# Kernel tuning notes

Measured on AMD Instinct MI355X. Metric: run time of the kernel, lower is better.

## Reference

```python
import jax, jax.numpy as jnp
import numpy as np
from jax import lax

H = 1024
B = 16384


def setup_inputs() -> dict:
    key = jax.random.key(0)
    ks = jax.random.split(key, 16)
    s = 1.0 / np.sqrt(H)
    inp = {
        "x": jax.random.normal(ks[0], (B, H), dtype=jnp.float32),
        "num_steps": 8,
        # operation_net: Linear(H,H) -> GELU -> Linear(H,5)
        "w_op1": jax.random.uniform(ks[1], (H, H), jnp.float32, -s, s),
        "b_op1": jax.random.uniform(ks[2], (H,), jnp.float32, -s, s),
        "w_op2": jax.random.uniform(ks[3], (H, 5), jnp.float32, -s, s),
        "b_op2": jax.random.uniform(ks[4], (5,), jnp.float32, -s, s),
        # number_net: Linear(H,H) -> GELU -> Linear(H,1)
        "w_num1": jax.random.uniform(ks[5], (H, H), jnp.float32, -s, s),
        "b_num1": jax.random.uniform(ks[6], (H,), jnp.float32, -s, s),
        "w_num2": jax.random.uniform(ks[7], (H, 1), jnp.float32, -s, s),
        "b_num2": jax.random.uniform(ks[8], (1,), jnp.float32, -s, s),
        # GRUCell params (PyTorch layout: [3H, H] with gate order r, z, n)
        "w_ih": jax.random.uniform(ks[9], (3 * H, H), jnp.float32, -s, s),
        "b_ih": jax.random.uniform(ks[10], (3 * H,), jnp.float32, -s, s),
        "w_hh": jax.random.uniform(ks[11], (3 * H, H), jnp.float32, -s, s),
        "b_hh": jax.random.uniform(ks[12], (3 * H,), jnp.float32, -s, s),
    }
    return inp


def _gelu(x):
    # PyTorch nn.GELU() default = exact (erf-based)
    return jax.nn.gelu(x, approximate=False)


def reference(x, num_steps, w_op1, b_op1, w_op2, b_op2,
              w_num1, b_num1, w_num2, b_num2,
              w_ih, b_ih, w_hh, b_hh):
    def step(h, _):
        # per-step heads (computed on the state BEFORE the GRU update)
        op_logits = _gelu(h @ w_op1 + b_op1) @ w_op2 + b_op2      # [B, 5]
        num_value = _gelu(h @ w_num1 + b_num1) @ w_num2 + b_num2  # [B, 1]
        # GRUCell with input == hidden == h
        gi = h @ w_ih.T + b_ih  # [B, 3H]
        gh = h @ w_hh.T + b_hh  # [B, 3H]
        i_r, i_z, i_n = jnp.split(gi, 3, axis=-1)
        h_r, h_z, h_n = jnp.split(gh, 3, axis=-1)
        r = jax.nn.sigmoid(i_r + h_r)
        z = jax.nn.sigmoid(i_z + h_z)
        n = jnp.tanh(i_n + r * h_n)
        h_new = (1.0 - z) * n + z * h
        return h_new, (op_logits, num_value, h)

    final_state, (ops, nums, states) = lax.scan(step, x, None, length=num_steps)
    # ops: [num_steps, B, 5], nums: [num_steps, B, 1], states: [num_steps, B, H]
    return final_state, ops, nums, states
```

## Files before the change

### kernel.cpp

```cpp
#include <hip/hip_runtime.h>
#include <hip/hip_bf16.h>
#include <math.h>

#define HDIM 1024
#define BROWS 16384
#define TSTEPS 8
#define NCOLS 6144
#define CCOLS 2048

typedef __bf16 bf16;
typedef __attribute__((ext_vector_type(8))) __bf16 bf16x8;
typedef __attribute__((ext_vector_type(4))) __bf16 bf16x4;
typedef __attribute__((ext_vector_type(4))) float f32x4;

__device__ __forceinline__ void async_ld16(void* lds, const void* g) {
  __builtin_amdgcn_global_load_lds((__attribute__((address_space(1))) void*)g,
                                   (__attribute__((address_space(3))) void*)lds,
                                   16, 0, 0);
}
__device__ __forceinline__ float gelu_exact(float x) {
  return 0.5f * x * (1.0f + erff(x * 0.70710678118654752f));
}
__device__ __forceinline__ float sigmoidf_(float x) {
  return 1.0f / (1.0f + __expf(-x));
}

__global__ void prep_trans(const float* __restrict__ w_op1, const float* __restrict__ w_num1,
                           bf16* __restrict__ Wcat) {
  __shared__ float tile[32][33];
  const float* src = blockIdx.z ? w_num1 : w_op1;
  const int cofs = blockIdx.z * 1024;
  const int kt = blockIdx.y * 32, nt = blockIdx.x * 32;
  const int tx = threadIdx.x, ty = threadIdx.y;
#pragma unroll
  for (int r = 0; r < 4; ++r) {
    int k = kt + ty + r * 8;
    tile[ty + r * 8][tx] = src[(size_t)k * HDIM + nt + tx];
  }
  __syncthreads();
#pragma unroll
  for (int r = 0; r < 4; ++r) {
    int n = nt + ty + r * 8;
    Wcat[(size_t)(cofs + n) * HDIM + kt + tx] = (bf16)tile[tx][ty + r * 8];
  }
}

__global__ void prep_gate(const float* __restrict__ w_ih, const float* __restrict__ w_hh,
                          bf16* __restrict__ Wcat) {
  const int np = blockIdx.x;
  const int k4 = threadIdx.x;
  const int g = np >> 6, sub = np & 63, kind = sub >> 4, idx = g * 16 + (sub & 15);
  const int r0 = (kind == 0) ? idx : (kind == 1) ? 1024 + idx : 2048 + idx;
  const float4* s1 = (const float4*)(w_ih + (size_t)r0 * HDIM);
  const float4* s2 = (const float4*)(w_hh + (size_t)r0 * HDIM);
  float4 v;
  if (kind <= 1) {
    float4 a = s1[k4], b = s2[k4];
    v.x = a.x + b.x; v.y = a.y + b.y; v.z = a.z + b.z; v.w = a.w + b.w;
  } else if (kind == 2) {
    v = s1[k4];
  } else {
    v = s2[k4];
  }
  bf16x4 o = {(bf16)v.x, (bf16)v.y, (bf16)v.z, (bf16)v.w};
  *(bf16x4*)(Wcat + (size_t)(2048 + np) * HDIM + k4 * 4) = o;
}

__global__ void prep_bias(const float* __restrict__ b_op1, const float* __restrict__ b_num1,
                          const float* __restrict__ b_ih, const float* __restrict__ b_hh,
                          float* __restrict__ bias) {
  int n = blockIdx.x * 256 + threadIdx.x;
  float v;
  if (n < 1024) v = b_op1[n];
  else if (n < 2048) v = b_num1[n - 1024];
  else {
    int np = n - 2048;
    int g = np >> 6, sub = np & 63, kind = sub >> 4, idx = g * 16 + (sub & 15);
    if (kind == 0) v = b_ih[idx] + b_hh[idx];
    else if (kind == 1) v = b_ih[1024 + idx] + b_hh[1024 + idx];
    else if (kind == 2) v = b_ih[2048 + idx];
    else v = b_hh[2048 + idx];
  }
  bias[n] = v;
}

__global__ void convert_x(const float* __restrict__ x, float* __restrict__ st0,
                          bf16* __restrict__ hbf) {
  size_t i = (size_t)blockIdx.x * 256 + threadIdx.x;
  float4 v = ((const float4*)x)[i];
  ((float4*)st0)[i] = v;
  bf16x4 b = {(bf16)v.x, (bf16)v.y, (bf16)v.z, (bf16)v.w};
  ((bf16x4*)hbf)[i] = b;
}

#define MFMA_BLK(I0, J0)                                                       \
  _Pragma("unroll") for (int i_ = 0; i_ < 4; ++i_)                             \
  _Pragma("unroll") for (int j_ = 0; j_ < 2; ++j_)                             \
  _Pragma("unroll") for (int k_ = 0; k_ < 2; ++k_)                             \
  acc[(I0) + i_][(J0) + j_] = __builtin_amdgcn_mfma_f32_16x16x32_bf16(         \
      afr[i_][k_], bfr[(J0) + j_][k_], acc[(I0) + i_][(J0) + j_], 0, 0, 0);

__global__ void __launch_bounds__(512) gemm_step(
    const bf16* __restrict__ A,
    const bf16* __restrict__ Bw,
    const float* __restrict__ bias,
    const float* __restrict__ h_old,
    float* __restrict__ h_new,
    bf16* __restrict__ hbf_n,
    bf16* __restrict__ C,
    int mt)
{
  __shared__ __align__(16) char smem[131072];
  bf16* const As0 = (bf16*)smem;
  bf16* const Bs0 = (bf16*)(smem + 32768);
  bf16* const As1 = (bf16*)(smem + 65536);
  bf16* const Bs1 = (bf16*)(smem + 98304);

  const int tid = threadIdx.x;
  const int wave = tid >> 6;
  const int lane = tid & 63;
  const int idx15 = lane & 15;
  const int quad = lane >> 4;
  const int wm = (wave >> 2) * 128;
  const int wn = (wave & 3) * 64;

  const int nwg = gridDim.x;
  const int cpx = nwg >> 3;
  const int wg = blockIdx.x;
  const int swz = (wg & 7) * cpx + (wg >> 3);
  const int tile_m = (swz % mt) * 256;
  const int tile_n = (swz / mt) * 256;

  const bf16* agp[2][2];
  const bf16* bgp[2][2];
  int lofs[2][2];
#pragma unroll
  for (int h = 0; h < 2; ++h)
#pragma unroll
    for (int q = 0; q < 2; ++q) {
      int p = h * 1024 + q * 512 + wave * 64 + lane;
      int pr = p >> 3;
      int c = (p & 7) ^ (pr & 7);
      int ma = ((pr >> 6) & 1) * 128 + (pr >> 7) * 64 + (pr & 63);
      int nb = ((pr >> 5) & 3) * 64 + (pr >> 7) * 32 + (pr & 31);
      agp[h][q] = A + (size_t)(tile_m + ma) * HDIM + c * 8;
      bgp[h][q] = Bw + (size_t)(tile_n + nb) * HDIM + c * 8;
      lofs[h][q] = (h * 1024 + q * 512 + wave * 64) * 8;
    }

  f32x4 acc[8][4] = {};
  bf16x8 afr[4][2], bfr[4][2];

  async_ld16(As0 + lofs[0][0], agp[0][0]);
  async_ld16(As0 + lofs[0][1], agp[0][1]);
  async_ld16(Bs0 + lofs[0][0], bgp[0][0]);
  async_ld16(Bs0 + lofs[0][1], bgp[0][1]);
  async_ld16(Bs0 + lofs[1][0], bgp[1][0]);
  async_ld16(Bs0 + lofs[1][1], bgp[1][1]);
  async_ld16(As0 + lofs[1][0], agp[1][0]);
  async_ld16(As0 + lofs[1][1], agp[1][1]);
  asm volatile("s_waitcnt vmcnt(4)" ::: "memory");
  __builtin_amdgcn_s_barrier();

  for (int t = 0; t < 16; ++t) {
    const int kn = ((t + 1) & 15) << 6;
    bf16* const Ac = (t & 1) ? As1 : As0;
    bf16* const Bc = (t & 1) ? Bs1 : Bs0;
    bf16* const An = (t & 1) ? As0 : As1;
    bf16* const Bn = (t & 1) ? Bs0 : Bs1;

#pragma unroll
    for (int i = 0; i < 4; ++i) {
      int pr = (wm >> 1) + i * 16 + idx15;
#pragma unroll
      for (int k = 0; k < 2; ++k)
        afr[i][k] = *(const bf16x8*)&Ac[(pr * 8 + ((k * 4 + quad) ^ (pr & 7))) * 8];
    }
#pragma unroll
    for (int j = 0; j < 2; ++j) {
      int pr = (wn >> 1) + j * 16 + idx15;
#pragma unroll
      for (int k = 0; k < 2; ++k)
        bfr[j][k] = *(const bf16x8*)&Bc[(pr * 8 + ((k * 4 + quad) ^ (pr & 7))) * 8];
    }
    async_ld16(An + lofs[0][0], agp[0][0] + kn);
    async_ld16(An + lofs[0][1], agp[0][1] + kn);
    __builtin_amdgcn_s_barrier();
    __builtin_amdgcn_s_setprio(1);
    MFMA_BLK(0, 0)
    __builtin_amdgcn_s_setprio(0);
    asm volatile("s_waitcnt vmcnt(4)" ::: "memory");
    __builtin_amdgcn_s_barrier();

#pragma unroll
    for (int j = 2; j < 4; ++j) {
      int pr = 128 + (wn >> 1) + (j & 1) * 16 + idx15;
#pragma unroll
      for (int k = 0; k < 2; ++k)
        bfr[j][k] = *(const bf16x8*)&Bc[(pr * 8 + ((k * 4 + quad) ^ (pr & 7))) * 8];
    }
    async_ld16(Bn + lofs[0][0], bgp[0][0] + kn);
    async_ld16(Bn + lofs[0][1], bgp[0][1] + kn);
    __builtin_amdgcn_s_barrier();
    __builtin_amdgcn_s_setprio(1);
    MFMA_BLK(0, 2)
    __builtin_amdgcn_s_setprio(0);
    asm volatile("s_waitcnt vmcnt(4)" ::: "memory");
    __builtin_amdgcn_s_barrier();

#pragma unroll
    for (int i = 0; i < 4; ++i) {
      int pr = 128 + (wm >> 1) + i * 16 + idx15;
#pragma unroll
      for (int k = 0; k < 2; ++k)
        afr[i][k] = *(const bf16x8*)&Ac[(pr * 8 + ((k * 4 + quad) ^ (pr & 7))) * 8];
    }
    async_ld16(Bn + lofs[1][0], bgp[1][0] + kn);
    async_ld16(Bn + lofs[1][1], bgp[1][1] + kn);
    __builtin_amdgcn_s_barrier();
    __builtin_amdgcn_s_setprio(1);
    MFMA_BLK(4, 0)
    __builtin_amdgcn_s_setprio(0);
    __builtin_amdgcn_s_barrier();

    async_ld16(An + lofs[1][0], agp[1][0] + kn);
    async_ld16(An + lofs[1][1], agp[1][1] + kn);
    __builtin_amdgcn_s_barrier();
    __builtin_amdgcn_s_setprio(1);
    MFMA_BLK(4, 2)
    __builtin_amdgcn_s_setprio(0);
    asm volatile("s_waitcnt vmcnt(4)" ::: "memory");
    __builtin_amdgcn_s_barrier();
  }

  asm volatile("s_waitcnt vmcnt(0)" ::: "memory");
  __builtin_amdgcn_s_barrier();

  if (tile_n < 2048) {
    bf16* Cs = (bf16*)smem;
#pragma unroll
    for (int j = 0; j < 4; ++j) {
      float bv = bias[tile_n + wn + j * 16 + idx15];
#pragma unroll
      for (int i = 0; i < 8; ++i) {
#pragma unroll
        for (int rr = 0; rr < 4; ++rr) {
          int ml = wm + i * 16 + quad * 4 + rr;
          float v = acc[i][j][rr] + bv;
          Cs[ml * 256 + wn + j * 16 + idx15] = (bf16)gelu_exact(v);
        }
      }
    }
    __syncthreads();
#pragma unroll
    for (int it = 0; it < 16; ++it) {
      int idx = it * 512 + tid;
      int ml = idx >> 5, c8 = (idx & 31) << 3;
      bf16x8 v = *(const bf16x8*)&Cs[ml * 256 + c8];
      *(bf16x8*)&C[(size_t)(tile_m + ml) * CCOLS + tile_n + c8] = v;
    }
  } else {
    float* Hs = (float*)smem;
    bf16* HBs = (bf16*)(smem + 65536);
    const int gb = (tile_n - 2048) >> 2;
    const int gl0 = wn >> 2;
    const int n0 = tile_n + wn;
    const float br = bias[n0 + idx15];
    const float bz = bias[n0 + 16 + idx15];
    const float bi = bias[n0 + 32 + idx15];
    const float bh = bias[n0 + 48 + idx15];
    const int gate = gb + gl0 + idx15;
#pragma unroll
    for (int i = 0; i < 8; ++i) {
#pragma unroll
      for (int rr = 0; rr < 4; ++rr) {
        int ml = wm + i * 16 + quad * 4 + rr;
        size_t row = (size_t)(tile_m + ml);
        float rg = sigmoidf_(acc[i][0][rr] + br);
        float zg = sigmoidf_(acc[i][1][rr] + bz);
        float ng = tanhf(acc[i][2][rr] + bi + rg * (acc[i][3][rr] + bh));
        float h = h_old[row * HDIM + gate];
        float v = (1.0f - zg) * ng + zg * h;
        Hs[ml * 64 + gl0 + idx15] = v;
        HBs[ml * 64 + gl0 + idx15] = (bf16)v;
      }
    }
    __syncthreads();
#pragma unroll
    for (int it = 0; it < 8; ++it) {
      int idx = it * 512 + tid;
      int ml = idx >> 4, g4 = (idx & 15) << 2;
      float4 v = *(const float4*)&Hs[ml * 64 + g4];
      *(float4*)&h_new[(size_t)(tile_m + ml) * HDIM + gb + g4] = v;
    }
#pragma unroll
    for (int it = 0; it < 4; ++it) {
      int idx = it * 512 + tid;
      int ml = idx >> 3, g8 = (idx & 7) << 3;
      bf16x8 v = *(const bf16x8*)&HBs[ml * 64 + g8];
      *(bf16x8*)&hbf_n[(size_t)(tile_m + ml) * HDIM + gb + g8] = v;
    }
  }
}

__global__ void __launch_bounds__(256) heads_step(
    const bf16* __restrict__ C, const float* __restrict__ w_op2,
    const float* __restrict__ b_op2, const float* __restrict__ w_num2,
    const float* __restrict__ b_num2, float* __restrict__ ops_t,
    float* __restrict__ nums_t, int row0) {
  const int wave = threadIdx.x >> 6;
  const int lane = threadIdx.x & 63;
  const int row = blockIdx.x * 4 + wave;
  const bf16* crow = C + (size_t)row * CCOLS;
  float a0 = 0, a1 = 0, a2 = 0, a3 = 0, a4 = 0, an = 0;
  for (int k = lane; k < HDIM; k += 64) {
    float hv = (float)crow[k];
    a0 += hv * w_op2[k * 5 + 0];
    a1 += hv * w_op2[k * 5 + 1];
    a2 += hv * w_op2[k * 5 + 2];
    a3 += hv * w_op2[k * 5 + 3];
    a4 += hv * w_op2[k * 5 + 4];
    an += (float)crow[HDIM + k] * w_num2[k];
  }
#pragma unroll
  for (int off = 32; off > 0; off >>= 1) {
    a0 += __shfl_down(a0, off);
    a1 += __shfl_down(a1, off);
    a2 += __shfl_down(a2, off);
    a3 += __shfl_down(a3, off);
    a4 += __shfl_down(a4, off);
    an += __shfl_down(an, off);
  }
  if (lane == 0) {
    size_t grow = (size_t)(row0 + row);
    ops_t[grow * 5 + 0] = a0 + b_op2[0];
    ops_t[grow * 5 + 1] = a1 + b_op2[1];
    ops_t[grow * 5 + 2] = a2 + b_op2[2];
    ops_t[grow * 5 + 3] = a3 + b_op2[3];
    ops_t[grow * 5 + 4] = a4 + b_op2[4];
    nums_t[grow] = an + b_num2[0];
  }
}

extern "C" void kernel_launch(void* const* d_in, const int* in_sizes, int n_in,
                              void* d_out, int out_size, void* d_ws, size_t ws_size,
                              hipStream_t stream) {
  const float* x      = (const float*)d_in[0];
  const float* w_op1  = (const float*)d_in[2];
  const float* b_op1  = (const float*)d_in[3];
  const float* w_op2  = (const float*)d_in[4];
  const float* b_op2  = (const float*)d_in[5];
  const float* w_num1 = (const float*)d_in[6];
  const float* b_num1 = (const float*)d_in[7];
  const float* w_num2 = (const float*)d_in[8];
  const float* b_num2 = (const float*)d_in[9];
  const float* w_ih   = (const float*)d_in[10];
  const float* b_ih   = (const float*)d_in[11];
  const float* w_hh   = (const float*)d_in[12];
  const float* b_hh   = (const float*)d_in[13];

  float* out = (float*)d_out;
  float* final_state = out;
  float* ops    = out + (size_t)BROWS * HDIM;
  float* nums   = ops + (size_t)TSTEPS * BROWS * 5;
  float* states = nums + (size_t)TSTEPS * BROWS;

  char* ws = (char*)d_ws;
  bf16* Wcat  = (bf16*)ws;
  float* bias = (float*)(ws + (size_t)NCOLS * HDIM * 2);
  bf16* hbf0  = (bf16*)(ws + (size_t)NCOLS * HDIM * 2 + NCOLS * 4);
  bf16* hbf1  = hbf0 + (size_t)BROWS * HDIM;
  char* cbase = (char*)(hbf1 + (size_t)BROWS * HDIM);
  bf16* C = (bf16*)cbase;
  size_t fixed = (size_t)(cbase - ws);

  int nch = 1;
  while (nch < 64 && fixed + (size_t)(BROWS / nch) * CCOLS * 2 > ws_size) nch *= 2;
  const int chunk = BROWS / nch;
  const int mt = chunk / 256;

  prep_trans<<<dim3(32, 32, 2), dim3(32, 8), 0, stream>>>(w_op1, w_num1, Wcat);
  prep_gate<<<4096, 256, 0, stream>>>(w_ih, w_hh, Wcat);
  prep_bias<<<NCOLS / 256, 256, 0, stream>>>(b_op1, b_num1, b_ih, b_hh, bias);
  convert_x<<<(BROWS * HDIM / 4) / 256, 256, 0, stream>>>(x, states, hbf0);

  for (int t = 0; t < TSTEPS; ++t) {
    float* st  = states + (size_t)t * BROWS * HDIM;
    float* stn = (t == TSTEPS - 1) ? final_state : states + (size_t)(t + 1) * BROWS * HDIM;
    float* ops_t  = ops + (size_t)t * BROWS * 5;
    float* nums_t = nums + (size_t)t * BROWS;
    const bf16* hin = (t & 1) ? hbf1 : hbf0;
    bf16* hout = (t & 1) ? hbf0 : hbf1;
    for (int c = 0; c < nch; ++c) {
      size_t r0 = (size_t)c * chunk;
      gemm_step<<<mt * (NCOLS / 256), 512, 0, stream>>>(
          hin + r0 * HDIM, Wcat, bias, st + r0 * HDIM, stn + r0 * HDIM,
          hout + r0 * HDIM, C, mt);
      heads_step<<<chunk / 4, 256, 0, stream>>>(C, w_op2, b_op2, w_num2, b_num2,
                                                ops_t, nums_t, (int)r0);
    }
  }
}
```

Baseline: 3.015 ms.

## Fuse second-layer heads into GEMM epilogue with atomic accumulation

The GELU head outputs are no longer written to a global C buffer and reduced by a separate heads kernel. Each GEMM tile now computes partial dot products with a transposed w_op2 (or w_num2) and atomically adds them into ops/nums, which are pre-initialised with the biases. This removes the C round trip, the extra kernel launches and the chunking. The change also pads the LDS epilogue strides to reduce bank conflicts and issues the async global-to-LDS prefetches before the fragment reads. In exchange it uses fp32 atomics, so summation order is nondeterministic, and the epilogue does extra per-thread work.

```diff
diff --git a/kernel.cpp b/kernel.cpp
--- a/kernel.cpp
+++ b/kernel.cpp
@@ -6,7 +6,11 @@
 #define BROWS 16384
 #define TSTEPS 8
 #define NCOLS 6144
-#define CCOLS 2048
+#define MT 64
+#define NT 24
+#define CS_STRIDE 264
+#define HS_STRIDE 68
+#define HB_STRIDE 72
 
 typedef __bf16 bf16;
 typedef __attribute__((ext_vector_type(8))) __bf16 bf16x8;
@@ -84,6 +88,20 @@
   bias[n] = v;
 }
 
+__global__ void prep_w2(const float* __restrict__ w_op2, float* __restrict__ wop2T) {
+  int idx = blockIdx.x * 256 + threadIdx.x;
+  int o = idx >> 10, c = idx & 1023;
+  wop2T[o * 1024 + c] = w_op2[c * 5 + o];
+}
+
+__global__ void init_heads(float* __restrict__ ops, float* __restrict__ nums,
+                           const float* __restrict__ b_op2, const float* __restrict__ b_num2) {
+  int idx = blockIdx.x * 256 + threadIdx.x;
+  const int N1 = TSTEPS * BROWS * 5;
+  if (idx < N1) ops[idx] = b_op2[idx % 5];
+  else nums[idx - N1] = b_num2[0];
+}
+
 __global__ void convert_x(const float* __restrict__ x, float* __restrict__ st0,
                           bf16* __restrict__ hbf) {
   size_t i = (size_t)blockIdx.x * 256 + threadIdx.x;
@@ -104,13 +122,15 @@
     const bf16* __restrict__ A,
     const bf16* __restrict__ Bw,
     const float* __restrict__ bias,
+    const float* __restrict__ wop2T,
+    const float* __restrict__ w_num2,
     const float* __restrict__ h_old,
     float* __restrict__ h_new,
     bf16* __restrict__ hbf_n,
-    bf16* __restrict__ C,
-    int mt)
+    float* __restrict__ ops_t,
+    float* __restrict__ nums_t)
 {
-  __shared__ __align__(16) char smem[131072];
+  __shared__ __align__(16) char smem[135168];
   bf16* const As0 = (bf16*)smem;
   bf16* const Bs0 = (bf16*)(smem + 32768);
   bf16* const As1 = (bf16*)(smem + 65536);
@@ -124,12 +144,10 @@
   const int wm = (wave >> 2) * 128;
   const int wn = (wave & 3) * 64;
 
-  const int nwg = gridDim.x;
-  const int cpx = nwg >> 3;
   const int wg = blockIdx.x;
-  const int swz = (wg & 7) * cpx + (wg >> 3);
-  const int tile_m = (swz % mt) * 256;
-  const int tile_n = (swz / mt) * 256;
+  const int swz = (wg & 7) * (MT * NT / 8) + (wg >> 3);
+  const int tile_m = (swz & (MT - 1)) * 256;
+  const int tile_n = (swz / MT) * 256;
 
   const bf16* agp[2][2];
   const bf16* bgp[2][2];
@@ -169,6 +187,8 @@
     bf16* const An = (t & 1) ? As0 : As1;
     bf16* const Bn = (t & 1) ? Bs0 : Bs1;
 
+    async_ld16(An + lofs[0][0], agp[0][0] + kn);
+    async_ld16(An + lofs[0][1], agp[0][1] + kn);
 #pragma unroll
     for (int i = 0; i < 4; ++i) {
       int pr = (wm >> 1) + i * 16 + idx15;
@@ -183,8 +203,6 @@
       for (int k = 0; k < 2; ++k)
         bfr[j][k] = *(const bf16x8*)&Bc[(pr * 8 + ((k * 4 + quad) ^ (pr & 7))) * 8];
     }
-    async_ld16(An + lofs[0][0], agp[0][0] + kn);
-    async_ld16(An + lofs[0][1], agp[0][1] + kn);
     __builtin_amdgcn_s_barrier();
     __builtin_amdgcn_s_setprio(1);
     MFMA_BLK(0, 0)
@@ -192,6 +210,8 @@
     asm volatile("s_waitcnt vmcnt(4)" ::: "memory");
     __builtin_amdgcn_s_barrier();
 
+    async_ld16(Bn + lofs[0][0], bgp[0][0] + kn);
+    async_ld16(Bn + lofs[0][1], bgp[0][1] + kn);
 #pragma unroll
     for (int j = 2; j < 4; ++j) {
       int pr = 128 + (wn >> 1) + (j & 1) * 16 + idx15;
@@ -199,8 +219,6 @@
       for (int k = 0; k < 2; ++k)
         bfr[j][k] = *(const bf16x8*)&Bc[(pr * 8 + ((k * 4 + quad) ^ (pr & 7))) * 8];
     }
-    async_ld16(Bn + lofs[0][0], bgp[0][0] + kn);
-    async_ld16(Bn + lofs[0][1], bgp[0][1] + kn);
     __builtin_amdgcn_s_barrier();
     __builtin_amdgcn_s_setprio(1);
     MFMA_BLK(0, 2)
@@ -208,6 +226,8 @@
     asm volatile("s_waitcnt vmcnt(4)" ::: "memory");
     __builtin_amdgcn_s_barrier();
 
+    async_ld16(Bn + lofs[1][0], bgp[1][0] + kn);
+    async_ld16(Bn + lofs[1][1], bgp[1][1] + kn);
 #pragma unroll
     for (int i = 0; i < 4; ++i) {
       int pr = 128 + (wm >> 1) + i * 16 + idx15;
@@ -215,8 +235,6 @@
       for (int k = 0; k < 2; ++k)
         afr[i][k] = *(const bf16x8*)&Ac[(pr * 8 + ((k * 4 + quad) ^ (pr & 7))) * 8];
     }
-    async_ld16(Bn + lofs[1][0], bgp[1][0] + kn);
-    async_ld16(Bn + lofs[1][1], bgp[1][1] + kn);
     __builtin_amdgcn_s_barrier();
     __builtin_amdgcn_s_setprio(1);
     MFMA_BLK(4, 0)
@@ -247,21 +265,61 @@
         for (int rr = 0; rr < 4; ++rr) {
           int ml = wm + i * 16 + quad * 4 + rr;
           float v = acc[i][j][rr] + bv;
-          Cs[ml * 256 + wn + j * 16 + idx15] = (bf16)gelu_exact(v);
+          Cs[ml * CS_STRIDE + wn + j * 16 + idx15] = (bf16)gelu_exact(v);
         }
       }
     }
     __syncthreads();
-#pragma unroll
-    for (int it = 0; it < 16; ++it) {
-      int idx = it * 512 + tid;
-      int ml = idx >> 5, c8 = (idx & 31) << 3;
-      bf16x8 v = *(const bf16x8*)&Cs[ml * 256 + c8];
-      *(bf16x8*)&C[(size_t)(tile_m + ml) * CCOLS + tile_n + c8] = v;
+    const int r = tid >> 1;
+    const int half = (tid & 1) * 128;
+    if (tile_n < 1024) {
+      const int colbase = tile_n + half;
+      float a0 = 0, a1 = 0, a2 = 0, a3 = 0, a4 = 0;
+#pragma unroll
+      for (int c8 = 0; c8 < 16; ++c8) {
+        bf16x8 v = *(const bf16x8*)&Cs[r * CS_STRIDE + half + c8 * 8];
+        float hv[8];
+#pragma unroll
+        for (int e = 0; e < 8; ++e) hv[e] = (float)v[e];
+        const float* wb = wop2T + colbase + c8 * 8;
+#pragma unroll
+        for (int e = 0; e < 8; ++e) {
+          a0 += hv[e] * wb[e];
+          a1 += hv[e] * wb[1024 + e];
+          a2 += hv[e] * wb[2048 + e];
+          a3 += hv[e] * wb[3072 + e];
+          a4 += hv[e] * wb[4096 + e];
+        }
+      }
+      a0 += __shfl_xor(a0, 1);
+      a1 += __shfl_xor(a1, 1);
+      a2 += __shfl_xor(a2, 1);
+      a3 += __shfl_xor(a3, 1);
+      a4 += __shfl_xor(a4, 1);
+      if (!(tid & 1)) {
+        float* dst = ops_t + (size_t)(tile_m + r) * 5;
+        atomicAdd(dst + 0, a0);
+        atomicAdd(dst + 1, a1);
+        atomicAdd(dst + 2, a2);
+        atomicAdd(dst + 3, a3);
+        atomicAdd(dst + 4, a4);
+      }
+    } else {
+      const int colbase = tile_n - 1024 + half;
+      float an = 0;
+#pragma unroll
+      for (int c8 = 0; c8 < 16; ++c8) {
+        bf16x8 v = *(const bf16x8*)&Cs[r * CS_STRIDE + half + c8 * 8];
+        const float* wb = w_num2 + colbase + c8 * 8;
+#pragma unroll
+        for (int e = 0; e < 8; ++e) an += (float)v[e] * wb[e];
+      }
+      an += __shfl_xor(an, 1);
+      if (!(tid & 1)) atomicAdd(nums_t + tile_m + r, an);
     }
   } else {
     float* Hs = (float*)smem;
-    bf16* HBs = (bf16*)(smem + 65536);
+    bf16* HBs = (bf16*)(smem + 256 * HS_STRIDE * 4);
     const int gb = (tile_n - 2048) >> 2;
     const int gl0 = wn >> 2;
     const int n0 = tile_n + wn;
@@ -281,8 +339,8 @@
         float ng = tanhf(acc[i][2][rr] + bi + rg * (acc[i][3][rr] + bh));
         float h = h_old[row * HDIM + gate];
         float v = (1.0f - zg) * ng + zg * h;
-        Hs[ml * 64 + gl0 + idx15] = v;
-        HBs[ml * 64 + gl0 + idx15] = (bf16)v;
+        Hs[ml * HS_STRIDE + gl0 + idx15] = v;
+        HBs[ml * HB_STRIDE + gl0 + idx15] = (bf16)v;
       }
     }
     __syncthreads();
@@ -290,55 +348,16 @@
     for (int it = 0; it < 8; ++it) {
       int idx = it * 512 + tid;
       int ml = idx >> 4, g4 = (idx & 15) << 2;
-      float4 v = *(const float4*)&Hs[ml * 64 + g4];
+      float4 v = *(const float4*)&Hs[ml * HS_STRIDE + g4];
       *(float4*)&h_new[(size_t)(tile_m + ml) * HDIM + gb + g4] = v;
     }
 #pragma unroll
     for (int it = 0; it < 4; ++it) {
       int idx = it * 512 + tid;
       int ml = idx >> 3, g8 = (idx & 7) << 3;
-      bf16x8 v = *(const bf16x8*)&HBs[ml * 64 + g8];
+      bf16x8 v = *(const bf16x8*)&HBs[ml * HB_STRIDE + g8];
       *(bf16x8*)&hbf_n[(size_t)(tile_m + ml) * HDIM + gb + g8] = v;
     }
-  }
-}
-
-__global__ void __launch_bounds__(256) heads_step(
-    const bf16* __restrict__ C, const float* __restrict__ w_op2,
-    const float* __restrict__ b_op2, const float* __restrict__ w_num2,
-    const float* __restrict__ b_num2, float* __restrict__ ops_t,
-    float* __restrict__ nums_t, int row0) {
-  const int wave = threadIdx.x >> 6;
-  const int lane = threadIdx.x & 63;
-  const int row = blockIdx.x * 4 + wave;
-  const bf16* crow = C + (size_t)row * CCOLS;
-  float a0 = 0, a1 = 0, a2 = 0, a3 = 0, a4 = 0, an = 0;
-  for (int k = lane; k < HDIM; k += 64) {
-    float hv = (float)crow[k];
-    a0 += hv * w_op2[k * 5 + 0];
-    a1 += hv * w_op2[k * 5 + 1];
-    a2 += hv * w_op2[k * 5 + 2];
-    a3 += hv * w_op2[k * 5 + 3];
-    a4 += hv * w_op2[k * 5 + 4];
-    an += (float)crow[HDIM + k] * w_num2[k];
-  }
-#pragma unroll
-  for (int off = 32; off > 0; off >>= 1) {
-    a0 += __shfl_down(a0, off);
-    a1 += __shfl_down(a1, off);
-    a2 += __shfl_down(a2, off);
-    a3 += __shfl_down(a3, off);
-    a4 += __shfl_down(a4, off);
-    an += __shfl_down(an, off);
-  }
-  if (lane == 0) {
-    size_t grow = (size_t)(row0 + row);
-    ops_t[grow * 5 + 0] = a0 + b_op2[0];
-    ops_t[grow * 5 + 1] = a1 + b_op2[1];
-    ops_t[grow * 5 + 2] = a2 + b_op2[2];
-    ops_t[grow * 5 + 3] = a3 + b_op2[3];
-    ops_t[grow * 5 + 4] = a4 + b_op2[4];
-    nums_t[grow] = an + b_num2[0];
   }
 }
 
@@ -366,22 +385,17 @@
   float* states = nums + (size_t)TSTEPS * BROWS;
 
   char* ws = (char*)d_ws;
-  bf16* Wcat  = (bf16*)ws;
-  float* bias = (float*)(ws + (size_t)NCOLS * HDIM * 2);
-  bf16* hbf0  = (bf16*)(ws + (size_t)NCOLS * HDIM * 2 + NCOLS * 4);
-  bf16* hbf1  = hbf0 + (size_t)BROWS * HDIM;
-  char* cbase = (char*)(hbf1 + (size_t)BROWS * HDIM);
-  bf16* C = (bf16*)cbase;
-  size_t fixed = (size_t)(cbase - ws);
-
-  int nch = 1;
-  while (nch < 64 && fixed + (size_t)(BROWS / nch) * CCOLS * 2 > ws_size) nch *= 2;
-  const int chunk = BROWS / nch;
-  const int mt = chunk / 256;
+  bf16* Wcat   = (bf16*)ws;
+  float* bias  = (float*)(ws + (size_t)NCOLS * HDIM * 2);
+  float* wop2T = bias + NCOLS;
+  bf16* hbf0   = (bf16*)(wop2T + 5 * HDIM);
+  bf16* hbf1   = hbf0 + (size_t)BROWS * HDIM;
 
   prep_trans<<<dim3(32, 32, 2), dim3(32, 8), 0, stream>>>(w_op1, w_num1, Wcat);
   prep_gate<<<4096, 256, 0, stream>>>(w_ih, w_hh, Wcat);
   prep_bias<<<NCOLS / 256, 256, 0, stream>>>(b_op1, b_num1, b_ih, b_hh, bias);
+  prep_w2<<<20, 256, 0, stream>>>(w_op2, wop2T);
+  init_heads<<<3072, 256, 0, stream>>>(ops, nums, b_op2, b_num2);
   convert_x<<<(BROWS * HDIM / 4) / 256, 256, 0, stream>>>(x, states, hbf0);
 
   for (int t = 0; t < TSTEPS; ++t) {
@@ -391,13 +405,7 @@
     float* nums_t = nums + (size_t)t * BROWS;
     const bf16* hin = (t & 1) ? hbf1 : hbf0;
     bf16* hout = (t & 1) ? hbf0 : hbf1;
-    for (int c = 0; c < nch; ++c) {
-      size_t r0 = (size_t)c * chunk;
-      gemm_step<<<mt * (NCOLS / 256), 512, 0, stream>>>(
-          hin + r0 * HDIM, Wcat, bias, st + r0 * HDIM, stn + r0 * HDIM,
-          hout + r0 * HDIM, C, mt);
-      heads_step<<<chunk / 4, 256, 0, stream>>>(C, w_op2, b_op2, w_num2, b_num2,
-                                                ops_t, nums_t, (int)r0);
-    }
-  }
-}
+    gemm_step<<<MT * NT, 512, 0, stream>>>(hin, Wcat, bias, wop2T, w_num2,
+                                           st, stn, hout, ops_t, nums_t);
+  }
+}
```

Result: slower. 3.114 ms (+3.3%).
